# Kernel tuning notes

Hardware: AMD Instinct MI355X
Metric: run time of the kernel (lower is better)

Reference implementation:

```python
import jax, jax.numpy as jnp
import numpy as np

EPS = 1e-5

def _layernorm_per_head(x, gamma, beta):
    # x: [b, h, L, d]; gamma, beta: [h, d] (distinct LayerNorm per head)
    mu = jnp.mean(x, axis=-1, keepdims=True)
    var = jnp.var(x, axis=-1, keepdims=True)
    xhat = (x - mu) * jax.lax.rsqrt(var + EPS)
    return xhat * gamma[None, :, None, :] + beta[None, :, None, :]

def setup_inputs() -> dict:
    key = jax.random.key(0)
    ks = jax.random.split(key, 10)
    b, nx, ny, nt = 2, 32, 32, 32
    cin, d, h = 128, 128, 8
    hd = h * d
    s_in = 1.0 / np.sqrt(cin)
    s_hd = 1.0 / np.sqrt(hd)
    return {
        "v": jax.random.normal(ks[0], (b, nx, ny, nt, cin), dtype=jnp.float32),
        "Wq_w": jax.random.normal(ks[1], (cin, hd), dtype=jnp.float32) * s_in,
        "Wq_b": jnp.zeros((hd,), dtype=jnp.float32),
        "Wk_w": jax.random.normal(ks[2], (cin, hd), dtype=jnp.float32) * s_in,
        "Wk_b": jnp.zeros((hd,), dtype=jnp.float32),
        "Wv_w": jax.random.normal(ks[3], (cin, hd), dtype=jnp.float32) * s_in,
        "Wv_b": jnp.zeros((hd,), dtype=jnp.float32),
        "Wo_w": jax.random.normal(ks[4], (hd, d), dtype=jnp.float32) * s_hd,
        "Wo_b": jnp.zeros((d,), dtype=jnp.float32),
        "lnk_g": jnp.ones((h, d), dtype=jnp.float32),
        "lnk_b": jnp.zeros((h, d), dtype=jnp.float32),
        "lnv_g": jnp.ones((h, d), dtype=jnp.float32),
        "lnv_b": jnp.zeros((h, d), dtype=jnp.float32),
    }

def reference(v, Wq_w, Wq_b, Wk_w, Wk_b, Wv_w, Wv_b, Wo_w, Wo_b,
              lnk_g, lnk_b, lnv_g, lnv_b):
    b, nx, ny, nt, cin = v.shape
    h, d = lnk_g.shape
    L = nx * ny * nt
    n = nx * ny  # NOTE: original divides by nx*ny only (not nt)
    x = v.reshape(b, L, cin)
    # projections -> [b, h, L, d]
    def proj(W, bias):
        y = x @ W + bias  # [b, L, h*d]
        return y.reshape(b, L, h, d).transpose(0, 2, 1, 3)
    Q = proj(Wq_w, Wq_b)
    K = proj(Wk_w, Wk_b)
    V = proj(Wv_w, Wv_b)
    K = _layernorm_per_head(K, lnk_g, lnk_b)
    V = _layernorm_per_head(V, lnv_g, lnv_b)
    # linear (Galerkin) attention: K^T V then Q (K^T V)
    attn_map = jnp.einsum('bhmd,bhmc->bhdc', K, V)      # [b, h, d, d]
    attn_out = jnp.einsum('bhld,bhdc->bhlc', Q, attn_map)  # [b, h, L, d]
    attn_out = attn_out.transpose(0, 2, 1, 3).reshape(b, L, h * d)
    out = (attn_out @ Wo_w + Wo_b) / n
    return out.reshape(b, nx, ny, nt, d)
```

## Files before the change

### kernel.cpp

```cpp
#include <hip/hip_runtime.h>
#include <stdint.h>

typedef unsigned short u16;
typedef unsigned int u32;
typedef __attribute__((ext_vector_type(8))) short s16x8;
typedef __attribute__((ext_vector_type(8))) __bf16 bf16x8;
typedef __attribute__((ext_vector_type(4))) float f32x4;
typedef __attribute__((ext_vector_type(4))) u16 u16x4;

#define L_TOT 32768
#define NCH 16

__device__ __forceinline__ u32 f2bf(float f){
  u32 u = __builtin_bit_cast(u32, f);
  return (u + 0x7FFFu + ((u >> 16) & 1u)) >> 16;
}
__device__ __forceinline__ u32 swz(u32 a){ return a ^ (((a >> 8) & 7u) << 4); }

__device__ __forceinline__ f32x4 mfma16(s16x8 a, s16x8 b, f32x4 c){
  return __builtin_amdgcn_mfma_f32_16x16x32_bf16(
      __builtin_bit_cast(bf16x8, a), __builtin_bit_cast(bf16x8, b), c, 0, 0, 0);
}

__device__ __forceinline__ void gload16(const void* g, void* l){
  __builtin_amdgcn_global_load_lds(
      (const __attribute__((address_space(1))) void*)g,
      (__attribute__((address_space(3))) void*)l, 16, 0, 0);
}

__device__ __forceinline__ u32 cvtpk(float lo, float hi){
  u32 r;
  asm("v_cvt_pk_bf16_f32 %0, %1, %2" : "=v"(r) : "v"(lo), "v"(hi));
  return r;
}

__device__ __forceinline__ float dpp_reduce16(float x){
  float y;
  asm("v_add_f32_dpp %0, %1, %1 row_ror:8 row_mask:0xf bank_mask:0xf"
      : "=&v"(y) : "v"(x));
  asm("v_add_f32_dpp %0, %1, %1 row_ror:4 row_mask:0xf bank_mask:0xf"
      : "=&v"(x) : "v"(y));
  asm("v_add_f32_dpp %0, %1, %1 quad_perm:[2,3,0,1] row_mask:0xf bank_mask:0xf"
      : "=&v"(y) : "v"(x));
  asm("v_add_f32_dpp %0, %1, %1 quad_perm:[1,0,3,2] row_mask:0xf bank_mask:0xf"
      : "=&v"(x) : "v"(y));
  return x;
}

__global__ void kprep(const float* __restrict__ v, const float* __restrict__ Wk,
                      const float* __restrict__ Wv, u16* __restrict__ X,
                      u16* __restrict__ WkT, u16* __restrict__ WvT){
  int tid = blockIdx.x * blockDim.x + threadIdx.x;
  int stride = gridDim.x * blockDim.x;
  for (int i = tid; i < 2097152; i += stride){
    float4 f = *((const float4*)v + i);
    u16x4 o; o.x = (u16)f2bf(f.x); o.y = (u16)f2bf(f.y); o.z = (u16)f2bf(f.z); o.w = (u16)f2bf(f.w);
    *((u16x4*)X + i) = o;
  }
  for (int i = tid; i < 131072; i += stride){
    int n = i >> 7, c = i & 127;
    WkT[i] = (u16)f2bf(Wk[c * 1024 + n]);
    WvT[i] = (u16)f2bf(Wv[c * 1024 + n]);
  }
}

__global__ __launch_bounds__(512, 2) void kattn(
    const u16* __restrict__ X, const u16* __restrict__ WkT, const u16* __restrict__ WvT,
    const float* __restrict__ bk, const float* __restrict__ bv,
    const float* __restrict__ gk, const float* __restrict__ bbk,
    const float* __restrict__ gv, const float* __restrict__ bbv,
    float* __restrict__ AM)
{
  extern __shared__ char smem[];
  char* sWk = smem;
  char* sWv = smem + 32768;
  char* sKT = smem + 65536;
  char* sVT = smem + 98304;

  const int tid = threadIdx.x;
  const int wid = tid >> 6, lane = tid & 63, g = lane >> 4, l15 = lane & 15;
  const int bh = blockIdx.x >> 4, grp = blockIdx.x & 15;
  const int b = bh >> 3, h = bh & 7;
  const bool isK = (wid < 4);
  const int w4 = wid & 3;

  {
    const char* gwk = (const char*)(WkT + h * 16384);
    const char* gwv = (const char*)(WvT + h * 16384);
    #pragma unroll
    for (int call = 0; call < 4; ++call){
      u32 o = (u32)(call * 8192 + wid * 1024 + lane * 16);
      gload16(gwk + swz(o), sWk + (call * 8192 + wid * 1024));
      gload16(gwv + swz(o), sWv + (call * 8192 + wid * 1024));
    }
  }
  const float* bias = isK ? bk : bv;
  const float* gam  = isK ? gk : gv;
  const float* beta = isK ? bbk : bbv;
  float br[8], gr[8], betar[8];
  #pragma unroll
  for (int nt = 0; nt < 8; ++nt){
    int idx = h * 128 + nt * 16 + l15;
    br[nt] = bias[idx]; gr[nt] = gam[idx]; betar[nt] = beta[idx];
  }
  asm volatile("s_waitcnt vmcnt(0)" ::: "memory");
  __builtin_amdgcn_s_barrier();

  f32x4 am[4][2];
  #pragma unroll
  for (int mt = 0; mt < 4; ++mt)
    #pragma unroll
    for (int nt = 0; nt < 2; ++nt) am[mt][nt] = f32x4{0.f, 0.f, 0.f, 0.f};

  const u16* Xb = X + (size_t)b * (L_TOT * 128);
  const char* sW = isK ? sWk : sWv;
  char* sT = isK ? sKT : sVT;

  auto pref = [&](s16x8 (&dst)[2][4], int chunk){
    int row0 = (grp * NCH + chunk) * 128;
    #pragma unroll
    for (int mt = 0; mt < 2; ++mt)
      #pragma unroll
      for (int ks = 0; ks < 4; ++ks){
        int r = row0 + w4 * 32 + mt * 16 + l15;
        dst[mt][ks] = *(const s16x8*)(Xb + (size_t)r * 128 + ks * 32 + g * 8);
      }
  };

  auto body = [&](const s16x8 (&af)[2][4]){
    f32x4 acc[2][8];
    #pragma unroll
    for (int mt = 0; mt < 2; ++mt)
      #pragma unroll
      for (int nt = 0; nt < 8; ++nt) acc[mt][nt] = f32x4{0.f, 0.f, 0.f, 0.f};
    #pragma unroll
    for (int ks = 0; ks < 4; ++ks){
      #pragma unroll
      for (int nt = 0; nt < 8; ++nt){
        u32 a = (u32)((nt * 16 + l15) * 256 + ks * 64 + g * 16);
        s16x8 bfr = *(const s16x8*)(sW + swz(a));
        acc[0][nt] = mfma16(af[0][ks], bfr, acc[0][nt]);
        acc[1][nt] = mfma16(af[1][ks], bfr, acc[1][nt]);
      }
    }
    #pragma unroll
    for (int mt = 0; mt < 2; ++mt){
      #pragma unroll
      for (int j = 0; j < 4; ++j){
        float s = 0.f, q = 0.f;
        float vv[8];
        #pragma unroll
        for (int nt = 0; nt < 8; ++nt){
          float t = acc[mt][nt][j] + br[nt];
          vv[nt] = t; s += t; q += t * t;
        }
        s = dpp_reduce16(s);
        q = dpp_reduce16(q);
        float mean = s * 0.0078125f;
        float var  = q * 0.0078125f - mean * mean;
        float rstd = rsqrtf(var + 1e-5f);
        #pragma unroll
        for (int nt = 0; nt < 8; ++nt)
          acc[mt][nt][j] = (vv[nt] - mean) * rstd * gr[nt] + betar[nt];
      }
      #pragma unroll
      for (int nt = 0; nt < 8; ++nt){
        int dk = nt * 16 + l15;
        int lc = w4 * 32 + mt * 16 + g * 4;
        u32 base = (u32)(dk * 256 + lc * 2);
        uint2 w; w.x = cvtpk(acc[mt][nt][0], acc[mt][nt][1]);
        w.y = cvtpk(acc[mt][nt][2], acc[mt][nt][3]);
        *(uint2*)(sT + swz(base)) = w;
      }
    }
    asm volatile("s_waitcnt lgkmcnt(0)" ::: "memory");
    __builtin_amdgcn_s_barrier();
    asm volatile("" ::: "memory");
    #pragma unroll
    for (int ks2 = 0; ks2 < 4; ++ks2){
      s16x8 a2[4], b2[2];
      #pragma unroll
      for (int mt2 = 0; mt2 < 4; ++mt2){
        int dk = (wid >> 2) * 64 + mt2 * 16 + l15;
        a2[mt2] = *(const s16x8*)(sKT + swz((u32)(dk * 256 + ks2 * 64 + g * 16)));
      }
      #pragma unroll
      for (int nt2 = 0; nt2 < 2; ++nt2){
        int dv = w4 * 32 + nt2 * 16 + l15;
        b2[nt2] = *(const s16x8*)(sVT + swz((u32)(dv * 256 + ks2 * 64 + g * 16)));
      }
      #pragma unroll
      for (int mt2 = 0; mt2 < 4; ++mt2)
        #pragma unroll
        for (int nt2 = 0; nt2 < 2; ++nt2)
          am[mt2][nt2] = mfma16(a2[mt2], b2[nt2], am[mt2][nt2]);
    }
    __builtin_amdgcn_s_barrier();
    asm volatile("" ::: "memory");
  };

  s16x8 af[2][4], afn[2][4];
  pref(af, 0);
  for (int it2 = 0; it2 < NCH; it2 += 2){
    pref(afn, it2 + 1);
    body(af);
    pref(af, (it2 + 2 < NCH) ? it2 + 2 : it2);
    body(afn);
  }

  float* AMbh = AM + (size_t)bh * 16384;
  #pragma unroll
  for (int mt2 = 0; mt2 < 4; ++mt2)
    #pragma unroll
    for (int nt2 = 0; nt2 < 2; ++nt2)
      #pragma unroll
      for (int j = 0; j < 4; ++j){
        int dk = (wid >> 2) * 64 + mt2 * 16 + g * 4 + j;
        int dv = w4 * 32 + nt2 * 16 + l15;
        atomicAdd(AMbh + dk * 128 + dv, am[mt2][nt2][j]);
      }
}

__global__ __launch_bounds__(256) void kfold(
    const float* __restrict__ AM, const float* __restrict__ Wo,
    const float* __restrict__ Wq, const float* __restrict__ Wq_b,
    const float* __restrict__ Wo_b,
    float* __restrict__ W4, float* __restrict__ c4)
{
  extern __shared__ float fsm[];
  float* sA = fsm;
  float* sS = fsm + 128 * 129;
  int blk = blockIdx.x;
  int bh = blk >> 2, eq = blk & 3;
  int b = bh >> 3, hs = bh & 7;
  int tid = threadIdx.x;

  for (int idx = tid; idx < 16384; idx += 256){
    int r = idx >> 7, c = idx & 127;
    sA[r * 129 + c] = AM[(size_t)bh * 16384 + idx];
  }
  for (int idx = tid; idx < 4096; idx += 256){
    int r = idx >> 5, c = idx & 31;
    sS[r * 33 + c] = Wo[(size_t)hs * 16384 + r * 128 + eq * 32 + c];
  }
  __syncthreads();

  int r0 = (tid >> 4) * 8, e0 = (tid & 15) * 2;
  float t8[8][2] = {};
  for (int c = 0; c < 128; ++c){
    float wv0 = sS[c * 33 + e0], wv1 = sS[c * 33 + e0 + 1];
    #pragma unroll
    for (int i = 0; i < 8; ++i){
      float a = sA[(r0 + i) * 129 + c];
      t8[i][0] += a * wv0; t8[i][1] += a * wv1;
    }
  }
  __syncthreads();
  #pragma unroll
  for (int i = 0; i < 8; ++i){
    sS[(r0 + i) * 33 + e0]     = t8[i][0];
    sS[(r0 + i) * 33 + e0 + 1] = t8[i][1];
  }
  for (int idx = tid; idx < 16384; idx += 256){
    int r = idx >> 7, c = idx & 127;
    sA[r * 129 + c] = Wq[(size_t)r * 1024 + hs * 128 + c];
  }
  __syncthreads();

  float a8[8][2] = {};
  for (int d = 0; d < 128; ++d){
    float t0 = sS[d * 33 + e0], t1 = sS[d * 33 + e0 + 1];
    #pragma unroll
    for (int i = 0; i < 8; ++i){
      float w = sA[(r0 + i) * 129 + d];
      a8[i][0] += w * t0; a8[i][1] += w * t1;
    }
  }
  const float inv_n = 0.0009765625f;
  #pragma unroll
  for (int i = 0; i < 8; ++i){
    atomicAdd(W4 + (size_t)b * 16384 + (r0 + i) * 128 + eq * 32 + e0,     a8[i][0] * inv_n);
    atomicAdd(W4 + (size_t)b * 16384 + (r0 + i) * 128 + eq * 32 + e0 + 1, a8[i][1] * inv_n);
  }
  if (tid < 32){
    float s = 0.f;
    for (int d = 0; d < 128; ++d) s += Wq_b[hs * 128 + d] * sS[d * 33 + tid];
    if (hs == 0) s += Wo_b[eq * 32 + tid];
    atomicAdd(c4 + b * 128 + eq * 32 + tid, s * inv_n);
  }
}

__global__ void kfold3(const float* __restrict__ W4, u16* __restrict__ W4T){
  int i = blockIdx.x * 256 + threadIdx.x;
  if (i >= 32768) return;
  int b = i >> 14, r = i & 16383, e = r >> 7, c = r & 127;
  W4T[i] = (u16)f2bf(W4[(size_t)b * 16384 + c * 128 + e]);
}

__global__ __launch_bounds__(256, 2) void kout(
    const u16* __restrict__ X, const u16* __restrict__ W4T,
    const float* __restrict__ c4, float* __restrict__ out)
{
  extern __shared__ char smem[];
  char* sX = smem; char* sW = smem + 32768;
  int tid = threadIdx.x, wid = tid >> 6, lane = tid & 63, g = lane >> 4, l15 = lane & 15;
  int blk = blockIdx.x; int b = blk >> 8, ch = blk & 255;
  const char* gx = (const char*)(X + ((size_t)b * L_TOT + ch * 128) * 128);
  const char* gw = (const char*)(W4T + (size_t)b * 16384);
  #pragma unroll
  for (int call = 0; call < 8; ++call){
    u32 o = (u32)(call * 4096 + wid * 1024 + lane * 16);
    gload16(gx + swz(o), sX + (call * 4096 + wid * 1024));
    gload16(gw + swz(o), sW + (call * 4096 + wid * 1024));
  }
  asm volatile("s_waitcnt vmcnt(0)" ::: "memory");
  __syncthreads();

  f32x4 acc[2][8];
  #pragma unroll
  for (int mt = 0; mt < 2; ++mt)
    #pragma unroll
    for (int nt = 0; nt < 8; ++nt) acc[mt][nt] = f32x4{0.f, 0.f, 0.f, 0.f};

  #pragma unroll
  for (int ks = 0; ks < 4; ++ks){
    s16x8 a0, a1;
    {
      int r = wid * 32 + l15;
      a0 = *(const s16x8*)(sX + swz((u32)(r * 256 + ks * 64 + g * 16)));
      a1 = *(const s16x8*)(sX + swz((u32)((r + 16) * 256 + ks * 64 + g * 16)));
    }
    #pragma unroll
    for (int nt = 0; nt < 8; ++nt){
      int e = nt * 16 + l15;
      s16x8 bfr = *(const s16x8*)(sW + swz((u32)(e * 256 + ks * 64 + g * 16)));
      acc[0][nt] = mfma16(a0, bfr, acc[0][nt]);
      acc[1][nt] = mfma16(a1, bfr, acc[1][nt]);
    }
  }
  float* ob = out + ((size_t)b * L_TOT + ch * 128) * 128;
  #pragma unroll
  for (int nt = 0; nt < 8; ++nt){
    float c4v = c4[b * 128 + nt * 16 + l15];
    #pragma unroll
    for (int mt = 0; mt < 2; ++mt)
      #pragma unroll
      for (int j = 0; j < 4; ++j){
        int r = wid * 32 + mt * 16 + g * 4 + j;
        ob[r * 128 + nt * 16 + l15] = acc[mt][nt][j] + c4v;
      }
  }
}

extern "C" void kernel_launch(void* const* d_in, const int* in_sizes, int n_in,
                              void* d_out, int out_size, void* d_ws, size_t ws_size,
                              hipStream_t stream){
  const float* v    = (const float*)d_in[0];
  const float* Wq_w = (const float*)d_in[1];
  const float* Wq_b = (const float*)d_in[2];
  const float* Wk_w = (const float*)d_in[3];
  const float* Wk_b = (const float*)d_in[4];
  const float* Wv_w = (const float*)d_in[5];
  const float* Wv_b = (const float*)d_in[6];
  const float* Wo_w = (const float*)d_in[7];
  const float* Wo_b = (const float*)d_in[8];
  const float* lnk_g = (const float*)d_in[9];
  const float* lnk_b = (const float*)d_in[10];
  const float* lnv_g = (const float*)d_in[11];
  const float* lnv_b = (const float*)d_in[12];

  char* ws = (char*)d_ws;
  u16*   X   = (u16*)  (ws);
  u16*   WkT = (u16*)  (ws + 16777216);
  u16*   WvT = (u16*)  (ws + 17039360);
  float* AM  = (float*)(ws + 17301504);
  float* W4  = (float*)(ws + 18350080);
  float* c4  = (float*)(ws + 18481152);
  u16*   W4T = (u16*)  (ws + 19530752);

  hipMemsetAsync(ws + 17301504, 0, 1180672, stream);

  hipLaunchKernelGGL(kprep, dim3(2048), dim3(256), 0, stream, v, Wk_w, Wv_w, X, WkT, WvT);

  (void)hipFuncSetAttribute((const void*)kattn,
                            hipFuncAttributeMaxDynamicSharedMemorySize, 131072);
  hipLaunchKernelGGL(kattn, dim3(256), dim3(512), 131072, stream,
                     X, WkT, WvT, Wk_b, Wv_b, lnk_g, lnk_b, lnv_g, lnv_b, AM);

  (void)hipFuncSetAttribute((const void*)kfold,
                            hipFuncAttributeMaxDynamicSharedMemorySize, 83968);
  hipLaunchKernelGGL(kfold, dim3(64), dim3(256), 83968, stream,
                     AM, Wo_w, Wq_w, Wq_b, Wo_b, W4, c4);
  hipLaunchKernelGGL(kfold3, dim3(128), dim3(256), 0, stream, W4, W4T);

  hipLaunchKernelGGL(kout, dim3(512), dim3(256), 65536, stream, X, W4T, c4, (float*)d_out);
}
```

Measured before the change: 148.0 us.

## Fold LayerNorm affine into post-pass and use fragment-major weight layouts

The LayerNorm gamma/beta application is moved out of the hot loop. The attention kernel now accumulates the raw normalized Gram matrix and per-column sums, and kfold reconstructs the affine-corrected K^T V algebraically. Weights are pre-permuted into MFMA fragment order so LDS reads need no swizzle, and K/V tiles are stored in fragment order. kout now reads X directly into registers instead of staging it through LDS, and allows higher occupancy. The risks are extra atomics for the sums and possible LDS bank conflicts from the unswizzled layouts.

Result: faster. 144.0 us (-2.7%).

```diff
diff --git a/kernel.cpp b/kernel.cpp
--- a/kernel.cpp
+++ b/kernel.cpp
@@ -6,6 +6,7 @@
 typedef __attribute__((ext_vector_type(8))) short s16x8;
 typedef __attribute__((ext_vector_type(8))) __bf16 bf16x8;
 typedef __attribute__((ext_vector_type(4))) float f32x4;
+typedef __attribute__((ext_vector_type(2))) float f32x2;
 typedef __attribute__((ext_vector_type(4))) u16 u16x4;
 
 #define L_TOT 32768
@@ -15,7 +16,6 @@
   u32 u = __builtin_bit_cast(u32, f);
   return (u + 0x7FFFu + ((u >> 16) & 1u)) >> 16;
 }
-__device__ __forceinline__ u32 swz(u32 a){ return a ^ (((a >> 8) & 7u) << 4); }
 
 __device__ __forceinline__ f32x4 mfma16(s16x8 a, s16x8 b, f32x4 c){
   return __builtin_amdgcn_mfma_f32_16x16x32_bf16(
@@ -49,7 +49,7 @@
 
 __global__ void kprep(const float* __restrict__ v, const float* __restrict__ Wk,
                       const float* __restrict__ Wv, u16* __restrict__ X,
-                      u16* __restrict__ WkT, u16* __restrict__ WvT){
+                      u16* __restrict__ WkF, u16* __restrict__ WvF){
   int tid = blockIdx.x * blockDim.x + threadIdx.x;
   int stride = gridDim.x * blockDim.x;
   for (int i = tid; i < 2097152; i += stride){
@@ -58,24 +58,25 @@
     *((u16x4*)X + i) = o;
   }
   for (int i = tid; i < 131072; i += stride){
-    int n = i >> 7, c = i & 127;
-    WkT[i] = (u16)f2bf(Wk[c * 1024 + n]);
-    WvT[i] = (u16)f2bf(Wv[c * 1024 + n]);
+    int e = i & 7, ln = (i >> 3) & 63, ks = (i >> 9) & 3, nt = (i >> 11) & 7, h = i >> 14;
+    int c = ks * 32 + (ln >> 4) * 8 + e;
+    int n = nt * 16 + (ln & 15);
+    int src = c * 1024 + h * 128 + n;
+    WkF[i] = (u16)f2bf(Wk[src]);
+    WvF[i] = (u16)f2bf(Wv[src]);
   }
 }
 
 __global__ __launch_bounds__(512, 2) void kattn(
-    const u16* __restrict__ X, const u16* __restrict__ WkT, const u16* __restrict__ WvT,
+    const u16* __restrict__ X, const u16* __restrict__ WkF, const u16* __restrict__ WvF,
     const float* __restrict__ bk, const float* __restrict__ bv,
-    const float* __restrict__ gk, const float* __restrict__ bbk,
-    const float* __restrict__ gv, const float* __restrict__ bbv,
-    float* __restrict__ AM)
+    float* __restrict__ G, float* __restrict__ KBar, float* __restrict__ VBar)
 {
   extern __shared__ char smem[];
-  char* sWk = smem;
-  char* sWv = smem + 32768;
-  char* sKT = smem + 65536;
-  char* sVT = smem + 98304;
+  char* sWK = smem;
+  char* sWV = smem + 32768;
+  char* sKF = smem + 65536;
+  char* sVF = smem + 98304;
 
   const int tid = threadIdx.x;
   const int wid = tid >> 6, lane = tid & 63, g = lane >> 4, l15 = lane & 15;
@@ -85,146 +86,138 @@
   const int w4 = wid & 3;
 
   {
-    const char* gwk = (const char*)(WkT + h * 16384);
-    const char* gwv = (const char*)(WvT + h * 16384);
-    #pragma unroll
-    for (int call = 0; call < 4; ++call){
-      u32 o = (u32)(call * 8192 + wid * 1024 + lane * 16);
-      gload16(gwk + swz(o), sWk + (call * 8192 + wid * 1024));
-      gload16(gwv + swz(o), sWv + (call * 8192 + wid * 1024));
+    const char* gwk = (const char*)(WkF + h * 16384);
+    const char* gwv = (const char*)(WvF + h * 16384);
+    #pragma unroll
+    for (int c = 0; c < 4; ++c){
+      u32 o = (u32)(c * 8192 + tid * 16);
+      gload16(gwk + o, sWK + o);
+      gload16(gwv + o, sWV + o);
     }
   }
   const float* bias = isK ? bk : bv;
-  const float* gam  = isK ? gk : gv;
-  const float* beta = isK ? bbk : bbv;
-  float br[8], gr[8], betar[8];
-  #pragma unroll
-  for (int nt = 0; nt < 8; ++nt){
-    int idx = h * 128 + nt * 16 + l15;
-    br[nt] = bias[idx]; gr[nt] = gam[idx]; betar[nt] = beta[idx];
-  }
+  float br[8];
+  #pragma unroll
+  for (int nt = 0; nt < 8; ++nt) br[nt] = bias[h * 128 + nt * 16 + l15];
+
   asm volatile("s_waitcnt vmcnt(0)" ::: "memory");
   __builtin_amdgcn_s_barrier();
 
+  const char* sW = isK ? sWK : sWV;
+  char* sT = isK ? sKF : sVF;
+  const u16* Xb = X + (size_t)b * (L_TOT * 128);
+
+  const u32 wread = (u32)(lane * 16);
+  char* stbase = sT + (((g >> 1) * 16 + l15) * 16 + (g & 1) * 8 + w4 * 1024);
+  const char* kfbase = sKF + lane * 16;
+  const char* vfbase = sVF + lane * 16;
+  const char* xlane = (const char*)Xb + (w4 * 32 + l15) * 256 + g * 16;
+
   f32x4 am[4][2];
   #pragma unroll
-  for (int mt = 0; mt < 4; ++mt)
-    #pragma unroll
-    for (int nt = 0; nt < 2; ++nt) am[mt][nt] = f32x4{0.f, 0.f, 0.f, 0.f};
-
-  const u16* Xb = X + (size_t)b * (L_TOT * 128);
-  const char* sW = isK ? sWk : sWv;
-  char* sT = isK ? sKT : sVT;
-
-  auto pref = [&](s16x8 (&dst)[2][4], int chunk){
-    int row0 = (grp * NCH + chunk) * 128;
-    #pragma unroll
-    for (int mt = 0; mt < 2; ++mt)
-      #pragma unroll
-      for (int ks = 0; ks < 4; ++ks){
-        int r = row0 + w4 * 32 + mt * 16 + l15;
-        dst[mt][ks] = *(const s16x8*)(Xb + (size_t)r * 128 + ks * 32 + g * 8);
-      }
-  };
-
-  auto body = [&](const s16x8 (&af)[2][4]){
-    f32x4 acc[2][8];
-    #pragma unroll
-    for (int mt = 0; mt < 2; ++mt)
-      #pragma unroll
-      for (int nt = 0; nt < 8; ++nt) acc[mt][nt] = f32x4{0.f, 0.f, 0.f, 0.f};
-    #pragma unroll
-    for (int ks = 0; ks < 4; ++ks){
-      #pragma unroll
-      for (int nt = 0; nt < 8; ++nt){
-        u32 a = (u32)((nt * 16 + l15) * 256 + ks * 64 + g * 16);
-        s16x8 bfr = *(const s16x8*)(sW + swz(a));
-        acc[0][nt] = mfma16(af[0][ks], bfr, acc[0][nt]);
-        acc[1][nt] = mfma16(af[1][ks], bfr, acc[1][nt]);
-      }
-    }
-    #pragma unroll
-    for (int mt = 0; mt < 2; ++mt){
+  for (int t = 0; t < 4; ++t)
+    #pragma unroll
+    for (int u2 = 0; u2 < 2; ++u2) am[t][u2] = f32x4{0.f, 0.f, 0.f, 0.f};
+  f32x2 kb2[8];
+  #pragma unroll
+  for (int nt = 0; nt < 8; ++nt) kb2[nt] = f32x2{0.f, 0.f};
+
+#define PREF(dst, it) { \
+  const char* p_ = xlane + (size_t)((grp * NCH + (it)) * 128) * 256; \
+  _Pragma("unroll") for (int mt_ = 0; mt_ < 2; ++mt_) \
+  _Pragma("unroll") for (int ks_ = 0; ks_ < 4; ++ks_) \
+    dst[mt_][ks_] = *(const s16x8*)(p_ + mt_ * 4096 + ks_ * 64); }
+
+#define BODY(F) { \
+    f32x4 acc[2][8]; \
+    _Pragma("unroll") for (int mt = 0; mt < 2; ++mt) \
+      _Pragma("unroll") for (int nt = 0; nt < 8; ++nt) acc[mt][nt] = f32x4{0.f,0.f,0.f,0.f}; \
+    _Pragma("unroll") for (int ks = 0; ks < 4; ++ks){ \
+      _Pragma("unroll") for (int nt = 0; nt < 8; ++nt){ \
+        s16x8 wf = *(const s16x8*)(sW + wread + (nt * 4 + ks) * 1024); \
+        acc[0][nt] = mfma16(F[0][ks], wf, acc[0][nt]); \
+        acc[1][nt] = mfma16(F[1][ks], wf, acc[1][nt]); \
+      } \
+    } \
+    _Pragma("unroll") for (int mt = 0; mt < 2; ++mt){ \
+      f32x4 sum = {0.f,0.f,0.f,0.f}, sq = {0.f,0.f,0.f,0.f}; \
+      _Pragma("unroll") for (int nt = 0; nt < 8; ++nt){ \
+        f32x4 t = acc[mt][nt] + f32x4{br[nt], br[nt], br[nt], br[nt]}; \
+        acc[mt][nt] = t; sum += t; sq += t * t; \
+      } \
+      f32x4 s4, ns4; \
+      _Pragma("unroll") for (int j = 0; j < 4; ++j){ \
+        float ssum = dpp_reduce16(sum[j]); \
+        float ssq  = dpp_reduce16(sq[j]); \
+        float mean = ssum * 0.0078125f; \
+        float var  = ssq * 0.0078125f - mean * mean; \
+        float rstd = rsqrtf(var + 1e-5f); \
+        s4[j] = rstd; ns4[j] = -mean * rstd; \
+      } \
+      _Pragma("unroll") for (int nt = 0; nt < 8; ++nt){ \
+        f32x4 t = acc[mt][nt] * s4 + ns4; \
+        kb2[nt] += f32x2{t.x, t.y} + f32x2{t.z, t.w}; \
+        uint2 w_; w_.x = cvtpk(t.x, t.y); w_.y = cvtpk(t.z, t.w); \
+        *(uint2*)(stbase + nt * 4096 + mt * 512) = w_; \
+      } \
+    } \
+    asm volatile("s_waitcnt lgkmcnt(0)" ::: "memory"); \
+    __builtin_amdgcn_s_barrier(); \
+    { \
+      const int dkt = (wid >> 2) * 4; \
+      _Pragma("unroll") for (int kk = 0; kk < 4; ++kk){ \
+        s16x8 a2[4], b2[2]; \
+        _Pragma("unroll") for (int t = 0; t < 4; ++t) \
+          a2[t] = *(const s16x8*)(kfbase + (dkt + t) * 4096 + kk * 1024); \
+        _Pragma("unroll") for (int u2 = 0; u2 < 2; ++u2) \
+          b2[u2] = *(const s16x8*)(vfbase + (w4 * 2 + u2) * 4096 + kk * 1024); \
+        _Pragma("unroll") for (int t = 0; t < 4; ++t) \
+          _Pragma("unroll") for (int u2 = 0; u2 < 2; ++u2) \
+            am[t][u2] = mfma16(a2[t], b2[u2], am[t][u2]); \
+      } \
+    } \
+    __builtin_amdgcn_s_barrier(); \
+  }
+
+  s16x8 af[2][4], afn[2][4];
+  PREF(af, 0);
+  #pragma unroll 1
+  for (int it2 = 0; it2 < NCH; it2 += 2){
+    PREF(afn, it2 + 1);
+    BODY(af);
+    PREF(af, (it2 + 2 < NCH) ? it2 + 2 : 0);
+    BODY(afn);
+  }
+#undef BODY
+#undef PREF
+
+  float* Gbh = G + (size_t)bh * 16384;
+  #pragma unroll
+  for (int t = 0; t < 4; ++t)
+    #pragma unroll
+    for (int u2 = 0; u2 < 2; ++u2)
       #pragma unroll
       for (int j = 0; j < 4; ++j){
-        float s = 0.f, q = 0.f;
-        float vv[8];
-        #pragma unroll
-        for (int nt = 0; nt < 8; ++nt){
-          float t = acc[mt][nt][j] + br[nt];
-          vv[nt] = t; s += t; q += t * t;
-        }
-        s = dpp_reduce16(s);
-        q = dpp_reduce16(q);
-        float mean = s * 0.0078125f;
-        float var  = q * 0.0078125f - mean * mean;
-        float rstd = rsqrtf(var + 1e-5f);
-        #pragma unroll
-        for (int nt = 0; nt < 8; ++nt)
-          acc[mt][nt][j] = (vv[nt] - mean) * rstd * gr[nt] + betar[nt];
+        int dk = (wid >> 2) * 64 + t * 16 + g * 4 + j;
+        int dv = w4 * 32 + u2 * 16 + l15;
+        atomicAdd(Gbh + dk * 128 + dv, am[t][u2][j]);
       }
-      #pragma unroll
-      for (int nt = 0; nt < 8; ++nt){
-        int dk = nt * 16 + l15;
-        int lc = w4 * 32 + mt * 16 + g * 4;
-        u32 base = (u32)(dk * 256 + lc * 2);
-        uint2 w; w.x = cvtpk(acc[mt][nt][0], acc[mt][nt][1]);
-        w.y = cvtpk(acc[mt][nt][2], acc[mt][nt][3]);
-        *(uint2*)(sT + swz(base)) = w;
-      }
-    }
-    asm volatile("s_waitcnt lgkmcnt(0)" ::: "memory");
-    __builtin_amdgcn_s_barrier();
-    asm volatile("" ::: "memory");
-    #pragma unroll
-    for (int ks2 = 0; ks2 < 4; ++ks2){
-      s16x8 a2[4], b2[2];
-      #pragma unroll
-      for (int mt2 = 0; mt2 < 4; ++mt2){
-        int dk = (wid >> 2) * 64 + mt2 * 16 + l15;
-        a2[mt2] = *(const s16x8*)(sKT + swz((u32)(dk * 256 + ks2 * 64 + g * 16)));
-      }
-      #pragma unroll
-      for (int nt2 = 0; nt2 < 2; ++nt2){
-        int dv = w4 * 32 + nt2 * 16 + l15;
-        b2[nt2] = *(const s16x8*)(sVT + swz((u32)(dv * 256 + ks2 * 64 + g * 16)));
-      }
-      #pragma unroll
-      for (int mt2 = 0; mt2 < 4; ++mt2)
-        #pragma unroll
-        for (int nt2 = 0; nt2 < 2; ++nt2)
-          am[mt2][nt2] = mfma16(a2[mt2], b2[nt2], am[mt2][nt2]);
-    }
-    __builtin_amdgcn_s_barrier();
-    asm volatile("" ::: "memory");
-  };
-
-  s16x8 af[2][4], afn[2][4];
-  pref(af, 0);
-  for (int it2 = 0; it2 < NCH; it2 += 2){
-    pref(afn, it2 + 1);
-    body(af);
-    pref(af, (it2 + 2 < NCH) ? it2 + 2 : it2);
-    body(afn);
-  }
-
-  float* AMbh = AM + (size_t)bh * 16384;
-  #pragma unroll
-  for (int mt2 = 0; mt2 < 4; ++mt2)
-    #pragma unroll
-    for (int nt2 = 0; nt2 < 2; ++nt2)
-      #pragma unroll
-      for (int j = 0; j < 4; ++j){
-        int dk = (wid >> 2) * 64 + mt2 * 16 + g * 4 + j;
-        int dv = w4 * 32 + nt2 * 16 + l15;
-        atomicAdd(AMbh + dk * 128 + dv, am[mt2][nt2][j]);
-      }
+  float* dstB = (isK ? KBar : VBar) + bh * 128;
+  #pragma unroll
+  for (int nt = 0; nt < 8; ++nt){
+    float kb = kb2[nt].x + kb2[nt].y;
+    kb += __shfl_xor(kb, 16);
+    kb += __shfl_xor(kb, 32);
+    if (g == 0) atomicAdd(dstB + nt * 16 + l15, kb);
+  }
 }
 
 __global__ __launch_bounds__(256) void kfold(
-    const float* __restrict__ AM, const float* __restrict__ Wo,
-    const float* __restrict__ Wq, const float* __restrict__ Wq_b,
-    const float* __restrict__ Wo_b,
+    const float* __restrict__ G, const float* __restrict__ KBar, const float* __restrict__ VBar,
+    const float* __restrict__ gk, const float* __restrict__ bbk,
+    const float* __restrict__ gv, const float* __restrict__ bbv,
+    const float* __restrict__ Wo, const float* __restrict__ Wq,
+    const float* __restrict__ Wq_b, const float* __restrict__ Wo_b,
     float* __restrict__ W4, float* __restrict__ c4)
 {
   extern __shared__ float fsm[];
@@ -235,9 +228,16 @@
   int b = bh >> 3, hs = bh & 7;
   int tid = threadIdx.x;
 
+  const float* gkh = gk + hs * 128; const float* bkh = bbk + hs * 128;
+  const float* gvh = gv + hs * 128; const float* bvh = bbv + hs * 128;
+  const float* kbh = KBar + bh * 128; const float* vbh = VBar + bh * 128;
+
   for (int idx = tid; idx < 16384; idx += 256){
     int r = idx >> 7, c = idx & 127;
-    sA[r * 129 + c] = AM[(size_t)bh * 16384 + idx];
+    float gg = G[(size_t)bh * 16384 + idx];
+    float am = gkh[r] * (gvh[c] * gg + kbh[r] * bvh[c])
+             + bkh[r] * (gvh[c] * vbh[c] + 32768.f * bvh[c]);
+    sA[r * 129 + c] = am;
   }
   for (int idx = tid; idx < 4096; idx += 256){
     int r = idx >> 5, c = idx & 31;
@@ -293,28 +293,37 @@
 __global__ void kfold3(const float* __restrict__ W4, u16* __restrict__ W4T){
   int i = blockIdx.x * 256 + threadIdx.x;
   if (i >= 32768) return;
-  int b = i >> 14, r = i & 16383, e = r >> 7, c = r & 127;
-  W4T[i] = (u16)f2bf(W4[(size_t)b * 16384 + c * 128 + e]);
-}
-
-__global__ __launch_bounds__(256, 2) void kout(
+  int b = i >> 14, o = i & 16383;
+  int e = o & 7, ln = (o >> 3) & 63, ks = (o >> 9) & 3, nt = (o >> 11) & 7;
+  int c = ks * 32 + (ln >> 4) * 8 + e;
+  int n = nt * 16 + (ln & 15);
+  W4T[i] = (u16)f2bf(W4[(size_t)b * 16384 + c * 128 + n]);
+}
+
+__global__ __launch_bounds__(256, 4) void kout(
     const u16* __restrict__ X, const u16* __restrict__ W4T,
     const float* __restrict__ c4, float* __restrict__ out)
 {
-  extern __shared__ char smem[];
-  char* sX = smem; char* sW = smem + 32768;
-  int tid = threadIdx.x, wid = tid >> 6, lane = tid & 63, g = lane >> 4, l15 = lane & 15;
-  int blk = blockIdx.x; int b = blk >> 8, ch = blk & 255;
-  const char* gx = (const char*)(X + ((size_t)b * L_TOT + ch * 128) * 128);
-  const char* gw = (const char*)(W4T + (size_t)b * 16384);
-  #pragma unroll
-  for (int call = 0; call < 8; ++call){
-    u32 o = (u32)(call * 4096 + wid * 1024 + lane * 16);
-    gload16(gx + swz(o), sX + (call * 4096 + wid * 1024));
-    gload16(gw + swz(o), sW + (call * 4096 + wid * 1024));
-  }
+  __shared__ char sW[32768];
+  const int tid = threadIdx.x, wid = tid >> 6, lane = tid & 63, g = lane >> 4, l15 = lane & 15;
+  const int blk = blockIdx.x, b = blk >> 8, ch = blk & 255;
+  {
+    const char* gw = (const char*)(W4T + (size_t)b * 16384);
+    #pragma unroll
+    for (int c = 0; c < 8; ++c){
+      u32 o = (u32)(c * 4096 + tid * 16);
+      gload16(gw + o, sW + o);
+    }
+  }
+  const char* xr = (const char*)(X + ((size_t)b * L_TOT + ch * 128 + wid * 32 + l15) * 128) + g * 16;
+  s16x8 af[2][4];
+  #pragma unroll
+  for (int mt = 0; mt < 2; ++mt)
+    #pragma unroll
+    for (int ks = 0; ks < 4; ++ks)
+      af[mt][ks] = *(const s16x8*)(xr + mt * 4096 + ks * 64);
   asm volatile("s_waitcnt vmcnt(0)" ::: "memory");
-  __syncthreads();
+  __builtin_amdgcn_s_barrier();
 
   f32x4 acc[2][8];
   #pragma unroll
@@ -322,33 +331,24 @@
     #pragma unroll
     for (int nt = 0; nt < 8; ++nt) acc[mt][nt] = f32x4{0.f, 0.f, 0.f, 0.f};
 
-  #pragma unroll
-  for (int ks = 0; ks < 4; ++ks){
-    s16x8 a0, a1;
-    {
-      int r = wid * 32 + l15;
-      a0 = *(const s16x8*)(sX + swz((u32)(r * 256 + ks * 64 + g * 16)));
-      a1 = *(const s16x8*)(sX + swz((u32)((r + 16) * 256 + ks * 64 + g * 16)));
+  const u32 wread = (u32)(lane * 16);
+  #pragma unroll
+  for (int ks = 0; ks < 4; ++ks)
+    #pragma unroll
+    for (int nt = 0; nt < 8; ++nt){
+      s16x8 wf = *(const s16x8*)(sW + wread + (nt * 4 + ks) * 1024);
+      acc[0][nt] = mfma16(af[0][ks], wf, acc[0][nt]);
+      acc[1][nt] = mfma16(af[1][ks], wf, acc[1][nt]);
     }
-    #pragma unroll
-    for (int nt = 0; nt < 8; ++nt){
-      int e = nt * 16 + l15;
-      s16x8 bfr = *(const s16x8*)(sW + swz((u32)(e * 256 + ks * 64 + g * 16)));
-      acc[0][nt] = mfma16(a0, bfr, acc[0][nt]);
-      acc[1][nt] = mfma16(a1, bfr, acc[1][nt]);
-    }
-  }
-  float* ob = out + ((size_t)b * L_TOT + ch * 128) * 128;
+  float* ob = out + ((size_t)b * L_TOT + ch * 128 + wid * 32) * 128;
   #pragma unroll
   for (int nt = 0; nt < 8; ++nt){
     float c4v = c4[b * 128 + nt * 16 + l15];
     #pragma unroll
     for (int mt = 0; mt < 2; ++mt)
       #pragma unroll
-      for (int j = 0; j < 4; ++j){
-        int r = wid * 32 + mt * 16 + g * 4 + j;
-        ob[r * 128 + nt * 16 + l15] = acc[mt][nt][j] + c4v;
-      }
+      for (int j = 0; j < 4; ++j)
+        ob[(mt * 16 + g * 4 + j) * 128 + nt * 16 + l15] = acc[mt][nt][j] + c4v;
   }
 }
 
@@ -370,28 +370,31 @@
   const float* lnv_b = (const float*)d_in[12];
 
   char* ws = (char*)d_ws;
-  u16*   X   = (u16*)  (ws);
-  u16*   WkT = (u16*)  (ws + 16777216);
-  u16*   WvT = (u16*)  (ws + 17039360);
-  float* AM  = (float*)(ws + 17301504);
-  float* W4  = (float*)(ws + 18350080);
-  float* c4  = (float*)(ws + 18481152);
-  u16*   W4T = (u16*)  (ws + 19530752);
-
-  hipMemsetAsync(ws + 17301504, 0, 1180672, stream);
-
-  hipLaunchKernelGGL(kprep, dim3(2048), dim3(256), 0, stream, v, Wk_w, Wv_w, X, WkT, WvT);
+  u16*   X    = (u16*)  (ws);
+  u16*   WkF  = (u16*)  (ws + 16777216);
+  u16*   WvF  = (u16*)  (ws + 17039360);
+  float* G    = (float*)(ws + 17301504);
+  float* KBar = (float*)(ws + 18350080);
+  float* VBar = (float*)(ws + 18358272);
+  float* W4   = (float*)(ws + 18366464);
+  float* c4   = (float*)(ws + 18497536);
+  u16*   W4T  = (u16*)  (ws + 18498560);
+
+  hipMemsetAsync(ws + 17301504, 0, 1197056, stream);
+
+  hipLaunchKernelGGL(kprep, dim3(2048), dim3(256), 0, stream, v, Wk_w, Wv_w, X, WkF, WvF);
 
   (void)hipFuncSetAttribute((const void*)kattn,
                             hipFuncAttributeMaxDynamicSharedMemorySize, 131072);
   hipLaunchKernelGGL(kattn, dim3(256), dim3(512), 131072, stream,
-                     X, WkT, WvT, Wk_b, Wv_b, lnk_g, lnk_b, lnv_g, lnv_b, AM);
+                     X, WkF, WvF, Wk_b, Wv_b, G, KBar, VBar);
 
   (void)hipFuncSetAttribute((const void*)kfold,
                             hipFuncAttributeMaxDynamicSharedMemorySize, 83968);
   hipLaunchKernelGGL(kfold, dim3(64), dim3(256), 83968, stream,
-                     AM, Wo_w, Wq_w, Wq_b, Wo_b, W4, c4);
+                     G, KBar, VBar, lnk_g, lnk_b, lnv_g, lnv_b,
+                     Wo_w, Wq_w, Wq_b, Wo_b, W4, c4);
   hipLaunchKernelGGL(kfold3, dim3(128), dim3(256), 0, stream, W4, W4T);
 
-  hipLaunchKernelGGL(kout, dim3(512), dim3(256), 65536, stream, X, W4T, c4, (float*)d_out);
-}
+  hipLaunchKernelGGL(kout, dim3(512), dim3(256), 0, stream, X, W4T, c4, (float*)d_out);
+}
```
